# Performance work log

Measured on AMD Instinct MI355X. Metric: run time of the kernel, lower is better.

Reference implementation:

```python
import jax, jax.numpy as jnp
import numpy as np
import math

B, N, D, H = 2, 64, 256, 8
DK = D // H


def setup_inputs() -> dict:
    key = jax.random.key(0)
    ks = jax.random.split(key, 12)
    s = 1.0 / math.sqrt(D)
    inp = {
        "state": jax.random.normal(ks[0], (B, N, N, D), dtype=jnp.float32),
        "mask": jnp.zeros((B, N, N, N), dtype=bool),
        "W_lk": jax.random.normal(ks[1], (D, D), dtype=jnp.float32) * s,
        "b_lk": jnp.zeros((D,), dtype=jnp.float32),
        "W_rk": jax.random.normal(ks[2], (D, D), dtype=jnp.float32) * s,
        "b_rk": jnp.zeros((D,), dtype=jnp.float32),
        "W_lv": jax.random.normal(ks[3], (D, D), dtype=jnp.float32) * s,
        "b_lv": jnp.zeros((D,), dtype=jnp.float32),
        "W_rv": jax.random.normal(ks[4], (D, D), dtype=jnp.float32) * s,
        "b_rv": jnp.zeros((D,), dtype=jnp.float32),
        "W_o": jax.random.normal(ks[5], (D, D), dtype=jnp.float32) * s,
        "b_o": jnp.zeros((D,), dtype=jnp.float32),
    }
    return inp


def _proj(x, W, b):
    # torch nn.Linear: x @ W.T + b, then view to heads
    y = jnp.einsum('bxyd,ed->bxye', x, W) + b
    return y.reshape(B, N, N, H, DK)


def reference(state, mask, W_lk, b_lk, W_rk, b_rk, W_lv, b_lv, W_rv, b_rv, W_o, b_o):
    left_k = _proj(state, W_lk, b_lk)   # [B,N,N,H,DK]
    right_k = _proj(state, W_rk, b_rk)
    left_v = _proj(state, W_lv, b_lv)
    right_v = _proj(state, W_rv, b_rv)

    # triangle-style scores over node triples (x, a, y): [B,N,N,N,H]
    scores = jnp.einsum('bxahd,bayhd->bxayh', left_k, right_k) / math.sqrt(DK)
    scores = jnp.where(mask[..., None], jnp.float32(-1000.0), scores)
    att = jax.nn.softmax(scores, axis=2)  # softmax over intermediate node a

    # val[b,x,a,y,h,d] = left_v[b,x,a,h,d] * right_v[b,a,y,h,d] (materialized as in torch)
    val = jnp.einsum('bxahd,bayhd->bxayhd', left_v, right_v)
    x = jnp.einsum('bxayh,bxayhd->bxyhd', att, val)  # sum over a
    x = x.reshape(B, N, N, D)
    return jnp.einsum('bxyd,ed->bxye', x, W_o) + b_o
```

## Files before the change

kernel.cpp:

```cpp
#include <hip/hip_runtime.h>

#define B 2
#define N 64
#define D 256
#define H 8
#define DK 32
#define M (B * N * N)

typedef __attribute__((ext_vector_type(8))) short bf16x8;
typedef __attribute__((ext_vector_type(4))) float f32x4;

#define PROJ_ELEMS (2097152)

__device__ __forceinline__ ushort f2b(float f) {
    union { float f; unsigned u; } v; v.f = f;
    unsigned r = v.u + 0x7fffu + ((v.u >> 16) & 1u);
    return (ushort)(r >> 16);
}
__device__ __forceinline__ float b2f(ushort u) {
    union { unsigned u; float f; } v; v.u = ((unsigned)u) << 16; return v.f;
}
__device__ __forceinline__ void cvt8(float4 raw, float* f) {
    const ushort* s = (const ushort*)&raw;
#pragma unroll
    for (int j = 0; j < 8; ++j) f[j] = b2f(s[j]);
}

__device__ __forceinline__ void glds16(const ushort* g, ushort* l) {
    __builtin_amdgcn_global_load_lds(
        (const __attribute__((address_space(1))) unsigned int*)g,
        (__attribute__((address_space(3))) unsigned int*)l, 16, 0, 0);
}

__global__ __launch_bounds__(256) void cast_all(const float* __restrict__ state,
                                                const float* __restrict__ W_lk, const float* __restrict__ W_rk,
                                                const float* __restrict__ W_lv, const float* __restrict__ W_rv,
                                                const float* __restrict__ W_o,
                                                const float* __restrict__ b_lk, const float* __restrict__ b_rk,
                                                const float* __restrict__ b_lv, const float* __restrict__ b_rv,
                                                const float* __restrict__ b_o,
                                                ushort* __restrict__ state_bf,
                                                ushort* __restrict__ Wcat,
                                                float* __restrict__ bias_cat) {
    const int gid = blockIdx.x * 256 + threadIdx.x;
    const float* Ws[5] = {W_lk, W_rk, W_lv, W_rv, W_o};
    const float* bs[5] = {b_lk, b_rk, b_lv, b_rv, b_o};

    if (gid < 1280) bias_cat[gid] = bs[gid >> 8][gid & 255];

    if (gid < 524288) {
        float4 v = *(const float4*)&state[(size_t)gid * 4];
        ushort4 o = {f2b(v.x), f2b(v.y), f2b(v.z), f2b(v.w)};
        *(ushort4*)&state_bf[(size_t)gid * 4] = o;
    } else {
        int u = gid - 524288;
        int row = u >> 6;
        int k4 = (u & 63) * 4;
        const float* W = Ws[row >> 8];
        float4 v = *(const float4*)&W[(size_t)(row & 255) * 256 + k4];
        ushort4 o = {f2b(v.x), f2b(v.y), f2b(v.z), f2b(v.w)};
        *(ushort4*)&Wcat[(size_t)row * 256 + k4] = o;
    }
}

template <int BF16OUT, int RELAYOUT>
__global__ __launch_bounds__(256) void gemm_mfma(const ushort* __restrict__ A,
                                                 const ushort* __restrict__ Bw,
                                                 const float* __restrict__ bias,
                                                 void* __restrict__ Cv, int ldc) {
    __shared__ __align__(16) ushort As[128 * 32];
    __shared__ __align__(16) ushort Bs[128 * 32];
    const int tid = threadIdx.x;
    const int lane = tid & 63;
    const int wave = tid >> 6;
    const int wm = (wave & 1) * 64;
    const int wn = (wave >> 1) * 64;
    const int row0 = blockIdx.x * 128;
    const int col0 = blockIdx.y * 128;

    const int lr = lane >> 2;
    const int lkq = (lane & 3) * 8;

    const ushort* gA0 = A + (size_t)(row0 + wave * 32 + lr) * 256 + lkq;
    const ushort* gA1 = gA0 + 16 * 256;
    const ushort* gB0 = Bw + (size_t)(col0 + wave * 32 + lr) * 256 + lkq;
    const ushort* gB1 = gB0 + 16 * 256;
    ushort* lA0 = &As[(wave * 32) * 32];
    ushort* lA1 = &As[(wave * 32 + 16) * 32];
    ushort* lB0 = &Bs[(wave * 32) * 32];
    ushort* lB1 = &Bs[(wave * 32 + 16) * 32];

    const int fr = lane & 15;
    const int fk = (lane >> 4) * 8;

    f32x4 acc[4][4] = {};

    for (int k0 = 0; k0 < 256; k0 += 32) {
        __syncthreads();
        glds16(gA0 + k0, lA0);
        glds16(gA1 + k0, lA1);
        glds16(gB0 + k0, lB0);
        glds16(gB1 + k0, lB1);
        __syncthreads();

        bf16x8 af[4], bf[4];
#pragma unroll
        for (int i = 0; i < 4; ++i)
            af[i] = *(const bf16x8*)&As[(wm + i * 16 + fr) * 32 + fk];
#pragma unroll
        for (int j = 0; j < 4; ++j)
            bf[j] = *(const bf16x8*)&Bs[(wn + j * 16 + fr) * 32 + fk];
#pragma unroll
        for (int i = 0; i < 4; ++i)
#pragma unroll
            for (int j = 0; j < 4; ++j)
                acc[i][j] = __builtin_amdgcn_mfma_f32_16x16x32_bf16(af[i], bf[j], acc[i][j], 0, 0, 0);
    }

#pragma unroll
    for (int j = 0; j < 4; ++j) {
        const int col = col0 + wn + j * 16 + (lane & 15);
        const float bv = bias[col];
#pragma unroll
        for (int i = 0; i < 4; ++i) {
            const int rbase = row0 + wm + i * 16 + (lane >> 4) * 4;
#pragma unroll
            for (int r = 0; r < 4; ++r) {
                float o = acc[i][j][r] + bv;
                if (RELAYOUT) {
                    const int row = rbase + r;
                    const int bb = row >> 12, rr = row & 4095;
                    const int proj = col >> 8, hh = (col >> 5) & 7, dk = col & 31;
                    ((ushort*)Cv)[(size_t)proj * PROJ_ELEMS +
                                  ((size_t)(bb * 8 + hh) * 4096 + rr) * 32 + dk] = f2b(o);
                } else if (BF16OUT) {
                    ((ushort*)Cv)[(size_t)(rbase + r) * ldc + col] = f2b(o);
                } else {
                    ((float*)Cv)[(size_t)(rbase + r) * ldc + col] = o;
                }
            }
        }
    }
}

__global__ __launch_bounds__(512) void fused_attn(const ushort* __restrict__ P,
                                                  const unsigned char* __restrict__ mask,
                                                  ushort* __restrict__ xbuf) {
    __shared__ __align__(16) float LVs[16 * 16 * 44];
    __shared__ __align__(16) float RVs[16 * 16 * 44];
    __shared__ __align__(16) float atts[16 * 16 * 20];
    __shared__ float mstate[16 * 20];
    __shared__ float lstate[16 * 20];
    __shared__ float alphas[16 * 20];

    const int bh = blockIdx.z;
    const int b = bh >> 3, h = bh & 7;
    const int x0 = blockIdx.x * 16, y0 = blockIdx.y * 16;
    const int tid = threadIdx.x;
    const int lane = tid & 63, wave = tid >> 6;

    const size_t HB = (size_t)bh * 4096 * 32;
    const ushort* PLK = P + HB;
    const ushort* PRK = P + (size_t)1 * PROJ_ELEMS + HB;
    const ushort* PLV = P + (size_t)2 * PROJ_ELEMS + HB;
    const ushort* PRV = P + (size_t)3 * PROJ_ELEMS + HB;

    const int y2 = (tid >> 4) & 3, dp = tid & 15;
    const int sx = tid >> 4, sy = tid & 15;
    if (tid < 256) {
        mstate[sx * 20 + sy] = -3.0e38f;
        lstate[sx * 20 + sy] = 0.0f;
    }

    float2 acc[2][4] = {};
    const float scale = 0.17677669529663687f;

    for (int ac = 0; ac < N; ac += 16) {
        __syncthreads();
#pragma unroll
        for (int it = 0; it < 2; ++it) {
            const int row = (tid >> 2) + it * 128;
            const int q = tid & 3;
            const int a = row >> 4, r = row & 15;
            float f[8];
            cvt8(*(const float4*)&PLV[((size_t)(x0 + r) * 64 + ac + a) * 32 + q * 8], f);
            *(float4*)&LVs[row * 44 + q * 8]     = make_float4(f[0], f[1], f[2], f[3]);
            *(float4*)&LVs[row * 44 + q * 8 + 4] = make_float4(f[4], f[5], f[6], f[7]);
            cvt8(*(const float4*)&PRV[((size_t)(ac + a) * 64 + y0 + r) * 32 + q * 8], f);
            *(float4*)&RVs[row * 44 + q * 8]     = make_float4(f[0], f[1], f[2], f[3]);
            *(float4*)&RVs[row * 44 + q * 8 + 4] = make_float4(f[4], f[5], f[6], f[7]);
        }
        {
            const int fr = lane & 15, fk = (lane >> 4) * 8;
            const int yq = lane & 15, xq = (lane >> 4) * 4;
#pragma unroll
            for (int aw = 0; aw < 2; ++aw) {
                const int a = wave * 2 + aw;
                bf16x8 af = *(const bf16x8*)&PLK[((size_t)(x0 + fr) * 64 + ac + a) * 32 + fk];
                bf16x8 bf = *(const bf16x8*)&PRK[((size_t)(ac + a) * 64 + y0 + fr) * 32 + fk];
                f32x4 s = {};
                s = __builtin_amdgcn_mfma_f32_16x16x32_bf16(af, bf, s, 0, 0, 0);
#pragma unroll
                for (int rr = 0; rr < 4; ++rr) {
                    const int x = xq + rr;
                    float sv = s[rr] * scale;
                    if (mask[((size_t)(b * N + x0 + x) * N + ac + a) * N + y0 + yq]) sv = -1000.0f;
                    atts[(a * 16 + x) * 20 + yq] = sv;
                }
            }
        }
        __syncthreads();

        if (tid < 256) {
            float s16[16];
            float mc = -3.0e38f;
#pragma unroll
            for (int a = 0; a < 16; ++a) {
                s16[a] = atts[(a * 16 + sx) * 20 + sy];
                mc = fmaxf(mc, s16[a]);
            }
            const float mold = mstate[sx * 20 + sy];
            const float mnew = fmaxf(mold, mc);
            const float alpha = __expf(mold - mnew);
            float ps = 0.0f;
#pragma unroll
            for (int a = 0; a < 16; ++a) {
                float p = __expf(s16[a] - mnew);
                atts[(a * 16 + sx) * 20 + sy] = p;
                ps += p;
            }
            lstate[sx * 20 + sy] = lstate[sx * 20 + sy] * alpha + ps;
            mstate[sx * 20 + sy] = mnew;
            alphas[sx * 20 + sy] = alpha;
        }
        __syncthreads();

#pragma unroll
        for (int i = 0; i < 2; ++i) {
            const int x = wave * 2 + i;
            float4 av = *(const float4*)&alphas[x * 20 + y2 * 4];
            const float* ap = (const float*)&av;
#pragma unroll
            for (int j = 0; j < 4; ++j) {
                acc[i][j].x *= ap[j];
                acc[i][j].y *= ap[j];
            }
        }
#pragma unroll
        for (int a = 0; a < 16; ++a) {
            float2 lv[2], rv[4];
#pragma unroll
            for (int i = 0; i < 2; ++i)
                lv[i] = *(const float2*)&LVs[(a * 16 + wave * 2 + i) * 44 + dp * 2];
#pragma unroll
            for (int j = 0; j < 4; ++j)
                rv[j] = *(const float2*)&RVs[(a * 16 + y2 * 4 + j) * 44 + dp * 2];
#pragma unroll
            for (int i = 0; i < 2; ++i) {
                float4 wv = *(const float4*)&atts[(a * 16 + wave * 2 + i) * 20 + y2 * 4];
                const float* wp = (const float*)&wv;
#pragma unroll
                for (int j = 0; j < 4; ++j) {
                    acc[i][j].x += (wp[j] * lv[i].x) * rv[j].x;
                    acc[i][j].y += (wp[j] * lv[i].y) * rv[j].y;
                }
            }
        }
    }

#pragma unroll
    for (int i = 0; i < 2; ++i) {
        const int x = wave * 2 + i;
        float4 lq = *(const float4*)&lstate[x * 20 + y2 * 4];
        const float* lp = (const float*)&lq;
#pragma unroll
        for (int j = 0; j < 4; ++j) {
            const float il = 1.0f / lp[j];
            ushort2 o = {f2b(acc[i][j].x * il), f2b(acc[i][j].y * il)};
            *(ushort2*)&xbuf[(((size_t)b * N + x0 + x) * N + y0 + y2 * 4 + j) * D + h * DK + 2 * dp] = o;
        }
    }
}

extern "C" void kernel_launch(void* const* d_in, const int* in_sizes, int n_in,
                              void* d_out, int out_size, void* d_ws, size_t ws_size,
                              hipStream_t stream) {
    const float* state = (const float*)d_in[0];
    const unsigned char* mask = (const unsigned char*)d_in[1];
    const float* W_lk = (const float*)d_in[2];
    const float* b_lk = (const float*)d_in[3];
    const float* W_rk = (const float*)d_in[4];
    const float* b_rk = (const float*)d_in[5];
    const float* W_lv = (const float*)d_in[6];
    const float* b_lv = (const float*)d_in[7];
    const float* W_rv = (const float*)d_in[8];
    const float* b_rv = (const float*)d_in[9];
    const float* W_o = (const float*)d_in[10];
    const float* b_o = (const float*)d_in[11];
    float* out = (float*)d_out;

    char* ws = (char*)d_ws;
    ushort* P_bf = (ushort*)ws;
    ws += (size_t)4 * PROJ_ELEMS * 2;
    float* bias_cat = (float*)ws;
    ws += 1280 * 4;
    ushort* state_bf = (ushort*)ws;
    ws += (size_t)M * D * 2;
    ushort* Wcat = (ushort*)ws;
    ws += (size_t)1280 * 256 * 2;
    ushort* xbuf_bf = (ushort*)ws;

    cast_all<<<2368, 256, 0, stream>>>(state, W_lk, W_rk, W_lv, W_rv, W_o,
                                       b_lk, b_rk, b_lv, b_rv, b_o,
                                       state_bf, Wcat, bias_cat);
    gemm_mfma<1, 1><<<dim3(M / 128, 8), 256, 0, stream>>>(state_bf, Wcat, bias_cat, P_bf, 1024);
    fused_attn<<<dim3(4, 4, B * H), 512, 0, stream>>>(P_bf, mask, xbuf_bf);
    gemm_mfma<0, 0><<<dim3(M / 128, 2), 256, 0, stream>>>(xbuf_bf, Wcat + 1024 * 256, bias_cat + 1024, out, 256);
}
```

Measured before the change: 124.5 us.

## Shrink attention tiles to 16x8 with 8-step chunks and 256-thread blocks

Reworks the fused triangle-attention kernel to use 16x8 output tiles per block with 256 threads, a reduction chunk of 8 intermediate nodes, and float4-wide per-thread accumulators over the DK dimension. This doubles the grid (512 blocks) to fill more compute units, and shrinks the shared-memory footprint. The score MFMA still computes 16 y columns but half are discarded, wasting some matrix work, and the number of sync-bounded chunk iterations doubles.

```diff
diff --git a/kernel.cpp b/kernel.cpp
--- a/kernel.cpp
+++ b/kernel.cpp
@@ -143,19 +143,19 @@
     }
 }
 
-__global__ __launch_bounds__(512) void fused_attn(const ushort* __restrict__ P,
+__global__ __launch_bounds__(256) void fused_attn(const ushort* __restrict__ P,
                                                   const unsigned char* __restrict__ mask,
                                                   ushort* __restrict__ xbuf) {
-    __shared__ __align__(16) float LVs[16 * 16 * 44];
-    __shared__ __align__(16) float RVs[16 * 16 * 44];
-    __shared__ __align__(16) float atts[16 * 16 * 20];
-    __shared__ float mstate[16 * 20];
-    __shared__ float lstate[16 * 20];
-    __shared__ float alphas[16 * 20];
+    __shared__ __align__(16) float LVs[128 * 44];
+    __shared__ __align__(16) float RVs[64 * 44];
+    __shared__ __align__(16) float atts[128 * 12];
+    __shared__ float mstate[16 * 10];
+    __shared__ float lstate[16 * 10];
+    __shared__ float alphas[16 * 10];
 
     const int bh = blockIdx.z;
     const int b = bh >> 3, h = bh & 7;
-    const int x0 = blockIdx.x * 16, y0 = blockIdx.y * 16;
+    const int x0 = blockIdx.x * 16, y0 = blockIdx.y * 8;
     const int tid = threadIdx.x;
     const int lane = tid & 63, wave = tid >> 6;
 
@@ -165,32 +165,35 @@
     const ushort* PLV = P + (size_t)2 * PROJ_ELEMS + HB;
     const ushort* PRV = P + (size_t)3 * PROJ_ELEMS + HB;
 
-    const int y2 = (tid >> 4) & 3, dp = tid & 15;
-    const int sx = tid >> 4, sy = tid & 15;
-    if (tid < 256) {
-        mstate[sx * 20 + sy] = -3.0e38f;
-        lstate[sx * 20 + sy] = 0.0f;
-    }
-
-    float2 acc[2][4] = {};
+    const int dg = tid & 7, yg = (tid >> 3) & 3, xg = tid >> 5;
+    const int sx = tid >> 3, sy = tid & 7;
+    if (tid < 128) {
+        mstate[sx * 10 + sy] = -3.0e38f;
+        lstate[sx * 10 + sy] = 0.0f;
+    }
+
+    f32x4 acc[2][2] = {};
     const float scale = 0.17677669529663687f;
 
-    for (int ac = 0; ac < N; ac += 16) {
-        __syncthreads();
-#pragma unroll
-        for (int it = 0; it < 2; ++it) {
-            const int row = (tid >> 2) + it * 128;
-            const int q = tid & 3;
-            const int a = row >> 4, r = row & 15;
-            float f[8];
-            cvt8(*(const float4*)&PLV[((size_t)(x0 + r) * 64 + ac + a) * 32 + q * 8], f);
-            *(float4*)&LVs[row * 44 + q * 8]     = make_float4(f[0], f[1], f[2], f[3]);
-            *(float4*)&LVs[row * 44 + q * 8 + 4] = make_float4(f[4], f[5], f[6], f[7]);
-            cvt8(*(const float4*)&PRV[((size_t)(ac + a) * 64 + y0 + r) * 32 + q * 8], f);
-            *(float4*)&RVs[row * 44 + q * 8]     = make_float4(f[0], f[1], f[2], f[3]);
-            *(float4*)&RVs[row * 44 + q * 8 + 4] = make_float4(f[4], f[5], f[6], f[7]);
-        }
+    for (int ac = 0; ac < N; ac += 8) {
+        __syncthreads();
         {
+            const int r = tid >> 1, q = tid & 1;
+            const int xL = r >> 3, aL = r & 7;
+            float f[16];
+            cvt8(*(const float4*)&PLV[((size_t)(x0 + xL) * 64 + ac + aL) * 32 + q * 16], f);
+            cvt8(*(const float4*)&PLV[((size_t)(x0 + xL) * 64 + ac + aL) * 32 + q * 16 + 8], f + 8);
+            *(float4*)&LVs[r * 44 + q * 16]      = make_float4(f[0], f[1], f[2], f[3]);
+            *(float4*)&LVs[r * 44 + q * 16 + 4]  = make_float4(f[4], f[5], f[6], f[7]);
+            *(float4*)&LVs[r * 44 + q * 16 + 8]  = make_float4(f[8], f[9], f[10], f[11]);
+            *(float4*)&LVs[r * 44 + q * 16 + 12] = make_float4(f[12], f[13], f[14], f[15]);
+
+            const int r2 = tid >> 2, q2 = tid & 3;
+            const int aR = r2 >> 3, yR = r2 & 7;
+            cvt8(*(const float4*)&PRV[((size_t)(ac + aR) * 64 + y0 + yR) * 32 + q2 * 8], f);
+            *(float4*)&RVs[r2 * 44 + q2 * 8]     = make_float4(f[0], f[1], f[2], f[3]);
+            *(float4*)&RVs[r2 * 44 + q2 * 8 + 4] = make_float4(f[4], f[5], f[6], f[7]);
+
             const int fr = lane & 15, fk = (lane >> 4) * 8;
             const int yq = lane & 15, xq = (lane >> 4) * 4;
 #pragma unroll
@@ -200,84 +203,78 @@
                 bf16x8 bf = *(const bf16x8*)&PRK[((size_t)(ac + a) * 64 + y0 + fr) * 32 + fk];
                 f32x4 s = {};
                 s = __builtin_amdgcn_mfma_f32_16x16x32_bf16(af, bf, s, 0, 0, 0);
-#pragma unroll
-                for (int rr = 0; rr < 4; ++rr) {
-                    const int x = xq + rr;
-                    float sv = s[rr] * scale;
-                    if (mask[((size_t)(b * N + x0 + x) * N + ac + a) * N + y0 + yq]) sv = -1000.0f;
-                    atts[(a * 16 + x) * 20 + yq] = sv;
+                if (yq < 8) {
+#pragma unroll
+                    for (int rr = 0; rr < 4; ++rr) {
+                        const int x = xq + rr;
+                        float sv = s[rr] * scale;
+                        if (mask[((size_t)(b * N + x0 + x) * N + ac + a) * N + y0 + yq]) sv = -1000.0f;
+                        atts[(a * 16 + x) * 12 + yq] = sv;
+                    }
                 }
             }
         }
         __syncthreads();
 
-        if (tid < 256) {
-            float s16[16];
+        if (tid < 128) {
+            float s8[8];
             float mc = -3.0e38f;
 #pragma unroll
-            for (int a = 0; a < 16; ++a) {
-                s16[a] = atts[(a * 16 + sx) * 20 + sy];
-                mc = fmaxf(mc, s16[a]);
-            }
-            const float mold = mstate[sx * 20 + sy];
+            for (int a = 0; a < 8; ++a) {
+                s8[a] = atts[(a * 16 + sx) * 12 + sy];
+                mc = fmaxf(mc, s8[a]);
+            }
+            const float mold = mstate[sx * 10 + sy];
             const float mnew = fmaxf(mold, mc);
             const float alpha = __expf(mold - mnew);
             float ps = 0.0f;
 #pragma unroll
-            for (int a = 0; a < 16; ++a) {
-                float p = __expf(s16[a] - mnew);
-                atts[(a * 16 + sx) * 20 + sy] = p;
+            for (int a = 0; a < 8; ++a) {
+                float p = __expf(s8[a] - mnew);
+                atts[(a * 16 + sx) * 12 + sy] = p;
                 ps += p;
             }
-            lstate[sx * 20 + sy] = lstate[sx * 20 + sy] * alpha + ps;
-            mstate[sx * 20 + sy] = mnew;
-            alphas[sx * 20 + sy] = alpha;
+            lstate[sx * 10 + sy] = lstate[sx * 10 + sy] * alpha + ps;
+            mstate[sx * 10 + sy] = mnew;
+            alphas[sx * 10 + sy] = alpha;
         }
         __syncthreads();
 
 #pragma unroll
         for (int i = 0; i < 2; ++i) {
-            const int x = wave * 2 + i;
-            float4 av = *(const float4*)&alphas[x * 20 + y2 * 4];
-            const float* ap = (const float*)&av;
-#pragma unroll
-            for (int j = 0; j < 4; ++j) {
-                acc[i][j].x *= ap[j];
-                acc[i][j].y *= ap[j];
-            }
-        }
-#pragma unroll
-        for (int a = 0; a < 16; ++a) {
-            float2 lv[2], rv[4];
+            float2 av = *(const float2*)&alphas[(xg * 2 + i) * 10 + yg * 2];
+            acc[i][0] *= av.x;
+            acc[i][1] *= av.y;
+        }
+#pragma unroll
+        for (int a = 0; a < 8; ++a) {
+            f32x4 lv[2], rv[2];
 #pragma unroll
             for (int i = 0; i < 2; ++i)
-                lv[i] = *(const float2*)&LVs[(a * 16 + wave * 2 + i) * 44 + dp * 2];
-#pragma unroll
-            for (int j = 0; j < 4; ++j)
-                rv[j] = *(const float2*)&RVs[(a * 16 + y2 * 4 + j) * 44 + dp * 2];
+                lv[i] = *(const f32x4*)&LVs[((xg * 2 + i) * 8 + a) * 44 + dg * 4];
+#pragma unroll
+            for (int j = 0; j < 2; ++j)
+                rv[j] = *(const f32x4*)&RVs[(a * 8 + yg * 2 + j) * 44 + dg * 4];
 #pragma unroll
             for (int i = 0; i < 2; ++i) {
-                float4 wv = *(const float4*)&atts[(a * 16 + wave * 2 + i) * 20 + y2 * 4];
-                const float* wp = (const float*)&wv;
-#pragma unroll
-                for (int j = 0; j < 4; ++j) {
-                    acc[i][j].x += (wp[j] * lv[i].x) * rv[j].x;
-                    acc[i][j].y += (wp[j] * lv[i].y) * rv[j].y;
-                }
+                float2 at = *(const float2*)&atts[(a * 16 + xg * 2 + i) * 12 + yg * 2];
+                acc[i][0] += (at.x * lv[i]) * rv[0];
+                acc[i][1] += (at.y * lv[i]) * rv[1];
             }
         }
     }
 
 #pragma unroll
     for (int i = 0; i < 2; ++i) {
-        const int x = wave * 2 + i;
-        float4 lq = *(const float4*)&lstate[x * 20 + y2 * 4];
+        const int x = xg * 2 + i;
+        float2 lq = *(const float2*)&lstate[x * 10 + yg * 2];
         const float* lp = (const float*)&lq;
 #pragma unroll
-        for (int j = 0; j < 4; ++j) {
+        for (int j = 0; j < 2; ++j) {
             const float il = 1.0f / lp[j];
-            ushort2 o = {f2b(acc[i][j].x * il), f2b(acc[i][j].y * il)};
-            *(ushort2*)&xbuf[(((size_t)b * N + x0 + x) * N + y0 + y2 * 4 + j) * D + h * DK + 2 * dp] = o;
+            f32x4 o = acc[i][j] * il;
+            ushort4 ob = {f2b(o[0]), f2b(o[1]), f2b(o[2]), f2b(o[3])};
+            *(ushort4*)&xbuf[(((size_t)b * N + x0 + x) * N + y0 + yg * 2 + j) * D + h * DK + dg * 4] = ob;
         }
     }
 }
@@ -314,6 +311,6 @@
                                        b_lk, b_rk, b_lv, b_rv, b_o,
                                        state_bf, Wcat, bias_cat);
     gemm_mfma<1, 1><<<dim3(M / 128, 8), 256, 0, stream>>>(state_bf, Wcat, bias_cat, P_bf, 1024);
-    fused_attn<<<dim3(4, 4, B * H), 512, 0, stream>>>(P_bf, mask, xbuf_bf);
+    fused_attn<<<dim3(4, 8, B * H), 256, 0, stream>>>(P_bf, mask, xbuf_bf);
     gemm_mfma<0, 0><<<dim3(M / 128, 2), 256, 0, stream>>>(xbuf_bf, Wcat + 1024 * 256, bias_cat + 1024, out, 256);
 }
```

Result: slower. 130.4 us (+4.7%).

## Prefetch next a-chunk's V tiles and score MFMAs into registers during accumulation

Applied to the files above, without the earlier changes.

Moves the global loads of the next chunk's left/right value tiles, along with the key loads, score MFMA and masking, into a register-held prefetch. That prefetch is issued right after the softmax barrier, so the next chunk's memory latency overlaps the current chunk's value-accumulation loop. At the top of each iteration the staged registers are converted to float and written to shared memory. This raises register pressure (plv/prv/sreg live across the accumulate loop), which could reduce occupancy.

```diff
diff --git a/kernel.cpp b/kernel.cpp
--- a/kernel.cpp
+++ b/kernel.cpp
@@ -175,38 +175,61 @@
     float2 acc[2][4] = {};
     const float scale = 0.17677669529663687f;
 
-    for (int ac = 0; ac < N; ac += 16) {
-        __syncthreads();
+    float4 plv[2], prv[2];
+    f32x4 sreg[2];
+
+    const int fr = lane & 15, fk = (lane >> 4) * 8;
+    const int yq = lane & 15, xq = (lane >> 4) * 4;
+
+    auto prefetch = [&](int ac) {
 #pragma unroll
         for (int it = 0; it < 2; ++it) {
             const int row = (tid >> 2) + it * 128;
             const int q = tid & 3;
             const int a = row >> 4, r = row & 15;
-            float f[8];
-            cvt8(*(const float4*)&PLV[((size_t)(x0 + r) * 64 + ac + a) * 32 + q * 8], f);
-            *(float4*)&LVs[row * 44 + q * 8]     = make_float4(f[0], f[1], f[2], f[3]);
-            *(float4*)&LVs[row * 44 + q * 8 + 4] = make_float4(f[4], f[5], f[6], f[7]);
-            cvt8(*(const float4*)&PRV[((size_t)(ac + a) * 64 + y0 + r) * 32 + q * 8], f);
-            *(float4*)&RVs[row * 44 + q * 8]     = make_float4(f[0], f[1], f[2], f[3]);
-            *(float4*)&RVs[row * 44 + q * 8 + 4] = make_float4(f[4], f[5], f[6], f[7]);
-        }
+            plv[it] = *(const float4*)&PLV[((size_t)(x0 + r) * 64 + ac + a) * 32 + q * 8];
+            prv[it] = *(const float4*)&PRV[((size_t)(ac + a) * 64 + y0 + r) * 32 + q * 8];
+        }
+#pragma unroll
+        for (int aw = 0; aw < 2; ++aw) {
+            const int a = wave * 2 + aw;
+            bf16x8 af = *(const bf16x8*)&PLK[((size_t)(x0 + fr) * 64 + ac + a) * 32 + fk];
+            bf16x8 bf = *(const bf16x8*)&PRK[((size_t)(ac + a) * 64 + y0 + fr) * 32 + fk];
+            f32x4 s = {};
+            s = __builtin_amdgcn_mfma_f32_16x16x32_bf16(af, bf, s, 0, 0, 0);
+#pragma unroll
+            for (int rr = 0; rr < 4; ++rr) {
+                float sv = s[rr] * scale;
+                if (mask[((size_t)(b * N + x0 + xq + rr) * N + ac + a) * N + y0 + yq]) sv = -1000.0f;
+                s[rr] = sv;
+            }
+            sreg[aw] = s;
+        }
+    };
+
+    prefetch(0);
+
+    for (int ac = 0; ac < N; ac += 16) {
+        __syncthreads();
         {
-            const int fr = lane & 15, fk = (lane >> 4) * 8;
-            const int yq = lane & 15, xq = (lane >> 4) * 4;
+#pragma unroll
+            for (int it = 0; it < 2; ++it) {
+                const int row = (tid >> 2) + it * 128;
+                const int q = tid & 3;
+                float f[8];
+                cvt8(plv[it], f);
+                *(float4*)&LVs[row * 44 + q * 8]     = make_float4(f[0], f[1], f[2], f[3]);
+                *(float4*)&LVs[row * 44 + q * 8 + 4] = make_float4(f[4], f[5], f[6], f[7]);
+                cvt8(prv[it], f);
+                *(float4*)&RVs[row * 44 + q * 8]     = make_float4(f[0], f[1], f[2], f[3]);
+                *(float4*)&RVs[row * 44 + q * 8 + 4] = make_float4(f[4], f[5], f[6], f[7]);
+            }
 #pragma unroll
             for (int aw = 0; aw < 2; ++aw) {
                 const int a = wave * 2 + aw;
-                bf16x8 af = *(const bf16x8*)&PLK[((size_t)(x0 + fr) * 64 + ac + a) * 32 + fk];
-                bf16x8 bf = *(const bf16x8*)&PRK[((size_t)(ac + a) * 64 + y0 + fr) * 32 + fk];
-                f32x4 s = {};
-                s = __builtin_amdgcn_mfma_f32_16x16x32_bf16(af, bf, s, 0, 0, 0);
-#pragma unroll
-                for (int rr = 0; rr < 4; ++rr) {
-                    const int x = xq + rr;
-                    float sv = s[rr] * scale;
-                    if (mask[((size_t)(b * N + x0 + x) * N + ac + a) * N + y0 + yq]) sv = -1000.0f;
-                    atts[(a * 16 + x) * 20 + yq] = sv;
-                }
+#pragma unroll
+                for (int rr = 0; rr < 4; ++rr)
+                    atts[(a * 16 + xq + rr) * 20 + yq] = sreg[aw][rr];
             }
         }
         __syncthreads();
@@ -234,6 +257,8 @@
             alphas[sx * 20 + sy] = alpha;
         }
         __syncthreads();
+
+        if (ac + 16 < N) prefetch(ac + 16);
 
 #pragma unroll
         for (int i = 0; i < 2; ++i) {
```

New measurement: 133.4 us. 7.1% more time.

## Fuse fp32-to-bf16 casts into GEMM tile loads and drop the cast kernel

Applied to the files above, without the earlier changes.

Removes the separate cast kernel and the bf16 copies of state and weights. The projection GEMM now loads fp32 state and weight tiles directly, converts them to bf16 in registers and stores them to shared memory. The output GEMM converts the fp32 W_o tiles the same way. This saves a launch and a round trip of the input through memory, but the tile loads go through registers instead of direct-to-LDS loads and fp32 A tiles are re-read by each column block.

```diff
diff --git a/kernel.cpp b/kernel.cpp
--- a/kernel.cpp
+++ b/kernel.cpp
@@ -32,41 +32,20 @@
         (__attribute__((address_space(3))) unsigned int*)l, 16, 0, 0);
 }
 
-__global__ __launch_bounds__(256) void cast_all(const float* __restrict__ state,
-                                                const float* __restrict__ W_lk, const float* __restrict__ W_rk,
-                                                const float* __restrict__ W_lv, const float* __restrict__ W_rv,
-                                                const float* __restrict__ W_o,
-                                                const float* __restrict__ b_lk, const float* __restrict__ b_rk,
-                                                const float* __restrict__ b_lv, const float* __restrict__ b_rv,
-                                                const float* __restrict__ b_o,
-                                                ushort* __restrict__ state_bf,
-                                                ushort* __restrict__ Wcat,
-                                                float* __restrict__ bias_cat) {
-    const int gid = blockIdx.x * 256 + threadIdx.x;
-    const float* Ws[5] = {W_lk, W_rk, W_lv, W_rv, W_o};
-    const float* bs[5] = {b_lk, b_rk, b_lv, b_rv, b_o};
-
-    if (gid < 1280) bias_cat[gid] = bs[gid >> 8][gid & 255];
-
-    if (gid < 524288) {
-        float4 v = *(const float4*)&state[(size_t)gid * 4];
-        ushort4 o = {f2b(v.x), f2b(v.y), f2b(v.z), f2b(v.w)};
-        *(ushort4*)&state_bf[(size_t)gid * 4] = o;
-    } else {
-        int u = gid - 524288;
-        int row = u >> 6;
-        int k4 = (u & 63) * 4;
-        const float* W = Ws[row >> 8];
-        float4 v = *(const float4*)&W[(size_t)(row & 255) * 256 + k4];
-        ushort4 o = {f2b(v.x), f2b(v.y), f2b(v.z), f2b(v.w)};
-        *(ushort4*)&Wcat[(size_t)row * 256 + k4] = o;
-    }
-}
-
-template <int BF16OUT, int RELAYOUT>
-__global__ __launch_bounds__(256) void gemm_mfma(const ushort* __restrict__ A,
-                                                 const ushort* __restrict__ Bw,
-                                                 const float* __restrict__ bias,
+__device__ __forceinline__ float4 pk8(float4 v0, float4 v1) {
+    union { ushort us[8]; float4 f4; } pk;
+    pk.us[0] = f2b(v0.x); pk.us[1] = f2b(v0.y); pk.us[2] = f2b(v0.z); pk.us[3] = f2b(v0.w);
+    pk.us[4] = f2b(v1.x); pk.us[5] = f2b(v1.y); pk.us[6] = f2b(v1.z); pk.us[7] = f2b(v1.w);
+    return pk.f4;
+}
+
+template <int AF32, int RELAYOUT>
+__global__ __launch_bounds__(256) void gemm_mfma(const float* __restrict__ A32,
+                                                 const ushort* __restrict__ A16,
+                                                 const float* __restrict__ Wb0, const float* __restrict__ Wb1,
+                                                 const float* __restrict__ Wb2, const float* __restrict__ Wb3,
+                                                 const float* __restrict__ bias0, const float* __restrict__ bias1,
+                                                 const float* __restrict__ bias2, const float* __restrict__ bias3,
                                                  void* __restrict__ Cv, int ldc) {
     __shared__ __align__(16) ushort As[128 * 32];
     __shared__ __align__(16) ushort Bs[128 * 32];
@@ -81,14 +60,20 @@
     const int lr = lane >> 2;
     const int lkq = (lane & 3) * 8;
 
-    const ushort* gA0 = A + (size_t)(row0 + wave * 32 + lr) * 256 + lkq;
-    const ushort* gA1 = gA0 + 16 * 256;
-    const ushort* gB0 = Bw + (size_t)(col0 + wave * 32 + lr) * 256 + lkq;
-    const ushort* gB1 = gB0 + 16 * 256;
+    const float* gA32a = A32 + (size_t)(row0 + wave * 32 + lr) * 256 + lkq;
+    const float* gA32b = gA32a + 16 * 256;
+    const ushort* gA16a = A16 + (size_t)(row0 + wave * 32 + lr) * 256 + lkq;
+    const ushort* gA16b = gA16a + 16 * 256;
+    const float* WB[4] = {Wb0, Wb1, Wb2, Wb3};
+    const int brow0 = col0 + wave * 32;
+    const float* gWa = WB[brow0 >> 8] + (size_t)((brow0 & 255) + lr) * 256 + lkq;
+    const float* gWb = gWa + 16 * 256;
+    ushort* lAa = &As[(wave * 32 + lr) * 32 + lkq];
+    ushort* lAb = lAa + 16 * 32;
     ushort* lA0 = &As[(wave * 32) * 32];
     ushort* lA1 = &As[(wave * 32 + 16) * 32];
-    ushort* lB0 = &Bs[(wave * 32) * 32];
-    ushort* lB1 = &Bs[(wave * 32 + 16) * 32];
+    ushort* lBa = &Bs[(wave * 32 + lr) * 32 + lkq];
+    ushort* lBb = lBa + 16 * 32;
 
     const int fr = lane & 15;
     const int fk = (lane >> 4) * 8;
@@ -96,11 +81,23 @@
     f32x4 acc[4][4] = {};
 
     for (int k0 = 0; k0 < 256; k0 += 32) {
-        __syncthreads();
-        glds16(gA0 + k0, lA0);
-        glds16(gA1 + k0, lA1);
-        glds16(gB0 + k0, lB0);
-        glds16(gB1 + k0, lB1);
+        float4 wa0 = *(const float4*)(gWa + k0), wa1 = *(const float4*)(gWa + k0 + 4);
+        float4 wb0 = *(const float4*)(gWb + k0), wb1 = *(const float4*)(gWb + k0 + 4);
+        float4 aa0, aa1, ab0, ab1;
+        if (AF32) {
+            aa0 = *(const float4*)(gA32a + k0); aa1 = *(const float4*)(gA32a + k0 + 4);
+            ab0 = *(const float4*)(gA32b + k0); ab1 = *(const float4*)(gA32b + k0 + 4);
+        }
+        __syncthreads();
+        if (AF32) {
+            *(float4*)lAa = pk8(aa0, aa1);
+            *(float4*)lAb = pk8(ab0, ab1);
+        } else {
+            glds16(gA16a + k0, lA0);
+            glds16(gA16b + k0, lA1);
+        }
+        *(float4*)lBa = pk8(wa0, wa1);
+        *(float4*)lBb = pk8(wb0, wb1);
         __syncthreads();
 
         bf16x8 af[4], bf[4];
@@ -117,10 +114,11 @@
                 acc[i][j] = __builtin_amdgcn_mfma_f32_16x16x32_bf16(af[i], bf[j], acc[i][j], 0, 0, 0);
     }
 
+    const float* BS[4] = {bias0, bias1, bias2, bias3};
 #pragma unroll
     for (int j = 0; j < 4; ++j) {
         const int col = col0 + wn + j * 16 + (lane & 15);
-        const float bv = bias[col];
+        const float bv = BS[col >> 8][col & 255];
 #pragma unroll
         for (int i = 0; i < 4; ++i) {
             const int rbase = row0 + wm + i * 16 + (lane >> 4) * 4;
@@ -133,8 +131,6 @@
                     const int proj = col >> 8, hh = (col >> 5) & 7, dk = col & 31;
                     ((ushort*)Cv)[(size_t)proj * PROJ_ELEMS +
                                   ((size_t)(bb * 8 + hh) * 4096 + rr) * 32 + dk] = f2b(o);
-                } else if (BF16OUT) {
-                    ((ushort*)Cv)[(size_t)(rbase + r) * ldc + col] = f2b(o);
                 } else {
                     ((float*)Cv)[(size_t)(rbase + r) * ldc + col] = o;
                 }
@@ -302,18 +298,13 @@
     char* ws = (char*)d_ws;
     ushort* P_bf = (ushort*)ws;
     ws += (size_t)4 * PROJ_ELEMS * 2;
-    float* bias_cat = (float*)ws;
-    ws += 1280 * 4;
-    ushort* state_bf = (ushort*)ws;
-    ws += (size_t)M * D * 2;
-    ushort* Wcat = (ushort*)ws;
-    ws += (size_t)1280 * 256 * 2;
     ushort* xbuf_bf = (ushort*)ws;
 
-    cast_all<<<2368, 256, 0, stream>>>(state, W_lk, W_rk, W_lv, W_rv, W_o,
-                                       b_lk, b_rk, b_lv, b_rv, b_o,
-                                       state_bf, Wcat, bias_cat);
-    gemm_mfma<1, 1><<<dim3(M / 128, 8), 256, 0, stream>>>(state_bf, Wcat, bias_cat, P_bf, 1024);
+    gemm_mfma<1, 1><<<dim3(M / 128, 8), 256, 0, stream>>>(
+        state, nullptr, W_lk, W_rk, W_lv, W_rv,
+        b_lk, b_rk, b_lv, b_rv, P_bf, 1024);
     fused_attn<<<dim3(4, 4, B * H), 512, 0, stream>>>(P_bf, mask, xbuf_bf);
-    gemm_mfma<0, 0><<<dim3(M / 128, 2), 256, 0, stream>>>(xbuf_bf, Wcat + 1024 * 256, bias_cat + 1024, out, 256);
-}
+    gemm_mfma<0, 0><<<dim3(M / 128, 2), 256, 0, stream>>>(
+        nullptr, xbuf_bf, W_o, W_o, W_o, W_o,
+        b_o, b_o, b_o, b_o, out, 256);
+}
```

New measurement: 129.5 us. 1.04x slower.
